# Optimization experiments

Measured on AMD Instinct MI355X. Metric: run time of the kernel, lower is better.

Reference implementation:

```python
import jax, jax.numpy as jnp
import numpy as np


def _bilinear_sample_zeros(img, px, py):
    """Bilinear sample img [B,C,H,W] at pixel coords px,py [B,...], zeros padding,
    align_corners=True semantics (coords are direct pixel indices)."""
    B, C, H, W = img.shape
    shp = px.shape
    px_f = px.reshape(B, -1)
    py_f = py.reshape(B, -1)
    x0 = jnp.floor(px_f)
    y0 = jnp.floor(py_f)
    fx = px_f - x0  # fractional offsets
    fy = py_f - y0
    x0i = x0.astype(jnp.int32)
    y0i = y0.astype(jnp.int32)
    img_flat = img.reshape(B, C, H * W)

    def corner(xi, yi, w):
        valid = ((xi >= 0) & (xi < W) & (yi >= 0) & (yi < H)).astype(img.dtype)
        xc = jnp.clip(xi, 0, W - 1)
        yc = jnp.clip(yi, 0, H - 1)
        idx = (yc * W + xc)[:, None, :]  # [B,1,N]
        v = jnp.take_along_axis(img_flat, idx, axis=2)  # [B,C,N]
        return v * (w * valid)[:, None, :]

    out = (corner(x0i, y0i, (1.0 - fx) * (1.0 - fy))
           + corner(x0i + 1, y0i, fx * (1.0 - fy))
           + corner(x0i, y0i + 1, (1.0 - fx) * fy)
           + corner(x0i + 1, y0i + 1, fx * fy))
    return out.reshape((B, C) + shp[1:])


def setup_inputs() -> dict:
    key = jax.random.key(0)
    k1, k2, k3 = jax.random.split(key, 3)
    B, C, H, W, D = 2, 32, 128, 256, 48
    x = jax.random.normal(k1, (B, C, H, W), dtype=jnp.float32)
    y = jax.random.normal(k2, (B, C, H, W), dtype=jnp.float32)
    disp = jax.random.uniform(k3, (B, D, H, W), dtype=jnp.float32) * 64.0
    return {"x": x, "y": y, "disp_range_samples": disp, "ndisp": D}


def reference(x, y, disp_range_samples, ndisp):
    B, C, H, W = x.shape
    # pixel coords of the warp: sample right image at (w - disparity, h)
    mw = jnp.arange(W, dtype=x.dtype).reshape(1, 1, 1, W)
    mh = jnp.arange(H, dtype=x.dtype).reshape(1, 1, H, 1)
    px = mw - disp_range_samples                       # [B, D, H, W]
    py = jnp.broadcast_to(mh, px.shape)                # [B, D, H, W]
    warped = _bilinear_sample_zeros(y, px, py)         # [B, C, D, H, W]
    # correlation mode: elementwise multiply with left features, mean over channels
    cost = (warped * x[:, :, None, :, :]).mean(axis=1)  # [B, D, H, W]
    return cost
```

## Files before the change

### kernel.cpp

```cpp
#include <hip/hip_runtime.h>

#define BB 2
#define CC 32
#define HH 128
#define WW 256
#define DD 48
#define HW (HH * WW)
#define NS 65
#define PAD 64
#define YROW (PAD + WW)


__global__ __launch_bounds__(1024) void cost_volume_kernel(
    const float* __restrict__ x, const float* __restrict__ y,
    const float* __restrict__ disp, float* __restrict__ out) {
  __shared__ float xs[CC * WW];
  __shared__ float ys[CC * YROW];
  __shared__ float corr[NS * WW];

  const int bx = blockIdx.x;
  const int b = bx >> 7;
  const int h = bx & 127;
  const int tid = threadIdx.x;

  const int gbase = (b * CC * HH + h) * WW;
  if (tid < 512) {
    int c = tid >> 4;
    int j = (tid & 15) << 2;
    *(float4*)&ys[c * YROW + j] = make_float4(0.f, 0.f, 0.f, 0.f);
  }
#pragma unroll
  for (int k = 0; k < 2; ++k) {
    int t = tid + (k << 10);
    int c = t >> 6;
    int w = (t & 63) << 2;
    float4 vx = *(const float4*)(x + gbase + c * HW + w);
    float4 vy = *(const float4*)(y + gbase + c * HW + w);
    *(float4*)&xs[c * WW + w] = vx;
    *(float4*)&ys[c * YROW + PAD + w] = vy;
  }
  __syncthreads();

  const int wid = tid >> 6;
  const int lane = tid & 63;
  const int w0 = lane << 2;

  if (wid < 8) {
    const int g = wid;
    float acc[8][4];
#pragma unroll
    for (int sl = 0; sl < 8; ++sl)
#pragma unroll
      for (int wj = 0; wj < 4; ++wj) acc[sl][wj] = 0.f;

    const int A = PAD + w0 - 8 * g - 8;
#pragma unroll 4
    for (int c = 0; c < CC; ++c) {
      float4 xv = *(const float4*)&xs[c * WW + w0];
      const float* yrow = &ys[c * YROW];
      float4 wv0 = *(const float4*)&yrow[A];
      float4 wv1 = *(const float4*)&yrow[A + 4];
      float4 wv2 = *(const float4*)&yrow[A + 8];
      float win[12] = {wv0.x, wv0.y, wv0.z, wv0.w, wv1.x, wv1.y,
                       wv1.z, wv1.w, wv2.x, wv2.y, wv2.z, wv2.w};
      float xr[4] = {xv.x, xv.y, xv.z, xv.w};
#pragma unroll
      for (int sl = 0; sl < 8; ++sl)
#pragma unroll
        for (int wj = 0; wj < 4; ++wj)
          acc[sl][wj] = fmaf(xr[wj], win[8 + wj - sl], acc[sl][wj]);
    }
#pragma unroll
    for (int sl = 0; sl < 8; ++sl)
      *(float4*)&corr[(8 * g + sl) * WW + w0] =
          make_float4(acc[sl][0], acc[sl][1], acc[sl][2], acc[sl][3]);
  } else if (wid == 8) {
    float acc[4] = {0.f, 0.f, 0.f, 0.f};
#pragma unroll 4
    for (int c = 0; c < CC; ++c) {
      float4 xv = *(const float4*)&xs[c * WW + w0];
      float4 yv = *(const float4*)&ys[c * YROW + w0];
      acc[0] = fmaf(xv.x, yv.x, acc[0]);
      acc[1] = fmaf(xv.y, yv.y, acc[1]);
      acc[2] = fmaf(xv.z, yv.z, acc[2]);
      acc[3] = fmaf(xv.w, yv.w, acc[3]);
    }
    *(float4*)&corr[64 * WW + w0] = make_float4(acc[0], acc[1], acc[2], acc[3]);
  }
  __syncthreads();

  const float inv_c = 1.0f / (float)CC;
  const float* dbase = disp + (b * DD * HH + h) * WW;
  float* obase = out + (b * DD * HH + h) * WW;
#pragma unroll
  for (int k = 0; k < (DD * WW) / 1024; ++k) {
    int idx = tid + (k << 10);
    int d = idx >> 8;
    int w = idx & 255;
    float dv = dbase[d * HW + w];
    float s0f = ceilf(dv);
    int i0 = (int)s0f;
    float fx = s0f - dv;
    int i1 = (i0 > 0) ? i0 - 1 : 0;
    float c0 = corr[i0 * WW + w];
    float c1 = corr[i1 * WW + w];
    obase[d * HW + w] = (c0 + fx * (c1 - c0)) * inv_c;
  }
}

extern "C" void kernel_launch(void* const* d_in, const int* in_sizes, int n_in,
                              void* d_out, int out_size, void* d_ws, size_t ws_size,
                              hipStream_t stream) {
  const float* x = (const float*)d_in[0];
  const float* y = (const float*)d_in[1];
  const float* disp = (const float*)d_in[2];
  float* out = (float*)d_out;
  cost_volume_kernel<<<BB * HH, 1024, 0, stream>>>(x, y, disp, out);
}
```

Before: 87.77 us.

## Spread correlation over all 16 waves and prefetch disparities before barrier

The correlation phase now uses all 16 wavefronts, each computing 4 shifts instead of 8 waves computing 8 shifts, with the zero-shift row folded into the last wave. The disparity values are loaded into registers right after the shared-memory fill, so their global-memory latency overlaps the correlation compute. This trades higher register pressure (48 prefetched floats per thread) for better load balance and latency hiding.

```diff
diff --git a/kernel.cpp b/kernel.cpp
--- a/kernel.cpp
+++ b/kernel.cpp
@@ -39,65 +39,66 @@
     *(float4*)&xs[c * WW + w] = vx;
     *(float4*)&ys[c * YROW + PAD + w] = vy;
   }
+
+  const float* dbase = disp + (b * DD * HH + h) * WW;
+  float dvp[(DD * WW) / 1024];
+#pragma unroll
+  for (int k = 0; k < (DD * WW) / 1024; ++k) {
+    int idx = tid + (k << 10);
+    dvp[k] = dbase[(idx >> 8) * HW + (idx & 255)];
+  }
   __syncthreads();
 
   const int wid = tid >> 6;
   const int lane = tid & 63;
   const int w0 = lane << 2;
+  const int sbase = wid << 2;
 
-  if (wid < 8) {
-    const int g = wid;
-    float acc[8][4];
+  float acc[4][4];
 #pragma unroll
-    for (int sl = 0; sl < 8; ++sl)
+  for (int sl = 0; sl < 4; ++sl)
 #pragma unroll
-      for (int wj = 0; wj < 4; ++wj) acc[sl][wj] = 0.f;
+    for (int wj = 0; wj < 4; ++wj) acc[sl][wj] = 0.f;
+  float a64[4] = {0.f, 0.f, 0.f, 0.f};
 
-    const int A = PAD + w0 - 8 * g - 8;
-#pragma unroll 4
-    for (int c = 0; c < CC; ++c) {
-      float4 xv = *(const float4*)&xs[c * WW + w0];
-      const float* yrow = &ys[c * YROW];
-      float4 wv0 = *(const float4*)&yrow[A];
-      float4 wv1 = *(const float4*)&yrow[A + 4];
-      float4 wv2 = *(const float4*)&yrow[A + 8];
-      float win[12] = {wv0.x, wv0.y, wv0.z, wv0.w, wv1.x, wv1.y,
-                       wv1.z, wv1.w, wv2.x, wv2.y, wv2.z, wv2.w};
-      float xr[4] = {xv.x, xv.y, xv.z, xv.w};
+  const int A = PAD + w0 - sbase - 4;
+#pragma unroll 2
+  for (int c = 0; c < CC; ++c) {
+    const float* yrow = &ys[c * YROW];
+    float4 xv = *(const float4*)&xs[c * WW + w0];
+    float4 wv0 = *(const float4*)&yrow[A];
+    float4 wv1 = *(const float4*)&yrow[A + 4];
+    float win[8] = {wv0.x, wv0.y, wv0.z, wv0.w, wv1.x, wv1.y, wv1.z, wv1.w};
+    float xr[4] = {xv.x, xv.y, xv.z, xv.w};
 #pragma unroll
-      for (int sl = 0; sl < 8; ++sl)
+    for (int sl = 0; sl < 4; ++sl)
 #pragma unroll
-        for (int wj = 0; wj < 4; ++wj)
-          acc[sl][wj] = fmaf(xr[wj], win[8 + wj - sl], acc[sl][wj]);
+      for (int wj = 0; wj < 4; ++wj)
+        acc[sl][wj] = fmaf(xr[wj], win[4 + wj - sl], acc[sl][wj]);
+    if (wid == 15) {
+      float4 yv = *(const float4*)&yrow[w0];
+      a64[0] = fmaf(xr[0], yv.x, a64[0]);
+      a64[1] = fmaf(xr[1], yv.y, a64[1]);
+      a64[2] = fmaf(xr[2], yv.z, a64[2]);
+      a64[3] = fmaf(xr[3], yv.w, a64[3]);
     }
+  }
 #pragma unroll
-    for (int sl = 0; sl < 8; ++sl)
-      *(float4*)&corr[(8 * g + sl) * WW + w0] =
-          make_float4(acc[sl][0], acc[sl][1], acc[sl][2], acc[sl][3]);
-  } else if (wid == 8) {
-    float acc[4] = {0.f, 0.f, 0.f, 0.f};
-#pragma unroll 4
-    for (int c = 0; c < CC; ++c) {
-      float4 xv = *(const float4*)&xs[c * WW + w0];
-      float4 yv = *(const float4*)&ys[c * YROW + w0];
-      acc[0] = fmaf(xv.x, yv.x, acc[0]);
-      acc[1] = fmaf(xv.y, yv.y, acc[1]);
-      acc[2] = fmaf(xv.z, yv.z, acc[2]);
-      acc[3] = fmaf(xv.w, yv.w, acc[3]);
-    }
-    *(float4*)&corr[64 * WW + w0] = make_float4(acc[0], acc[1], acc[2], acc[3]);
-  }
+  for (int sl = 0; sl < 4; ++sl)
+    *(float4*)&corr[(sbase + sl) * WW + w0] =
+        make_float4(acc[sl][0], acc[sl][1], acc[sl][2], acc[sl][3]);
+  if (wid == 15)
+    *(float4*)&corr[64 * WW + w0] = make_float4(a64[0], a64[1], a64[2], a64[3]);
   __syncthreads();
 
   const float inv_c = 1.0f / (float)CC;
-  const float* dbase = disp + (b * DD * HH + h) * WW;
   float* obase = out + (b * DD * HH + h) * WW;
 #pragma unroll
   for (int k = 0; k < (DD * WW) / 1024; ++k) {
     int idx = tid + (k << 10);
     int d = idx >> 8;
     int w = idx & 255;
-    float dv = dbase[d * HW + w];
+    float dv = dvp[k];
     float s0f = ceilf(dv);
     int i0 = (int)s0f;
     float fx = s0f - dv;
```

New measurement: 91.81 us. +4.6%, slower.
